# Optimization experiments

Hardware: AMD Instinct MI355X
Metric: run time of the kernel (lower is better)

## Reference

```python
import jax, jax.numpy as jnp
import numpy as np
import math

D_K = 64

def setup_inputs() -> dict:
    key = jax.random.key(0)
    kq, kk, kv, km = jax.random.split(key, 4)
    B, H, S, D = 4, 16, 2048, D_K
    Q = jax.random.normal(kq, (B, H, S, D), dtype=jnp.float32)
    K = jax.random.normal(kk, (B, H, S, D), dtype=jnp.float32)
    V = jax.random.normal(kv, (B, H, S, D), dtype=jnp.float32)
    attn_mask = jax.random.randint(km, (1, 1, S, S), 0, 2, dtype=jnp.int32)
    return {"Q": Q, "K": K, "V": V, "attn_mask": attn_mask}

def reference(Q, K, V, attn_mask):
    # scores: [B,H,S,S]
    scores = jnp.einsum('bhqd,bhkd->bhqk', Q, K) / math.sqrt(D_K)
    scores = jnp.where(attn_mask == 0, jnp.float32(-1e9), scores)
    attn = jax.nn.softmax(scores, axis=-1)
    context = jnp.einsum('bhqk,bhkd->bhqd', attn, V)
    return (context, attn)
```

## Files before the change

kernel.cpp:

```cpp
#include <hip/hip_runtime.h>
#include <hip/hip_bf16.h>
#include <stdint.h>

#define S_LEN 2048
#define DH    64
#define NBH   64
#define QR    128
#define KTI   64
#define NT    (S_LEN / KTI)
#define NTHR  512
#define SCALE2 (0.125f * 1.44269504f)
#define EXPB2  23.0f

using f32x4   = __attribute__((ext_vector_type(4))) float;
using short8v = __attribute__((ext_vector_type(8))) short;
using short4v = __attribute__((ext_vector_type(4))) short;

__device__ __forceinline__ short f2bf(float f) {
    union { float f; uint32_t u; } v; v.f = f;
    uint32_t u = v.u;
    return (short)((u + 0x7FFFu + ((u >> 16) & 1u)) >> 16);
}


__global__ void pack_mask_kernel(const int* __restrict__ mask, uint32_t* __restrict__ pmL) {
    int tid = blockIdx.x * 256 + threadIdx.x;
    int c  = tid & 15;
    int t  = (tid >> 4) & (NT - 1);
    int q4 = tid >> 9;
    uint32_t bits = 0;
    #pragma unroll
    for (int r = 0; r < 4; ++r)
        #pragma unroll
        for (int n = 0; n < 4; ++n) {
            int q = q4 * 4 + r;
            int k = t * KTI + n * 16 + c;
            if (mask[q * S_LEN + k]) bits |= 1u << (r * 4 + n);
        }
    pmL[tid] = bits;
}

__global__ void conv_k_kernel(const float* __restrict__ K, uint16_t* __restrict__ Kb) {
    size_t i = ((size_t)blockIdx.x * 256 + threadIdx.x) * 8;
    float4 a = *reinterpret_cast<const float4*>(K + i);
    float4 b = *reinterpret_cast<const float4*>(K + i + 4);
    short8v o;
    o[0] = f2bf(a.x); o[1] = f2bf(a.y); o[2] = f2bf(a.z); o[3] = f2bf(a.w);
    o[4] = f2bf(b.x); o[5] = f2bf(b.y); o[6] = f2bf(b.z); o[7] = f2bf(b.w);
    *reinterpret_cast<short8v*>(Kb + i) = o;
}

__global__ void trans_v_kernel(const float* __restrict__ V, uint16_t* __restrict__ Vt) {
    __shared__ short Ts[DH][72];
    int bh = blockIdx.x;
    int t  = blockIdx.y;
    const float* Vb = V + ((size_t)bh * S_LEN + t * KTI) * DH;
    int tid = threadIdx.x;
    #pragma unroll
    for (int i = 0; i < 4; ++i) {
        int lin = tid + i * 256;
        int row = lin >> 4;
        int c4  = (lin & 15) << 2;
        float4 v4 = *reinterpret_cast<const float4*>(Vb + row * DH + c4);
        Ts[c4 + 0][row] = f2bf(v4.x);
        Ts[c4 + 1][row] = f2bf(v4.y);
        Ts[c4 + 2][row] = f2bf(v4.z);
        Ts[c4 + 3][row] = f2bf(v4.w);
    }
    __syncthreads();
    #pragma unroll
    for (int i = 0; i < 2; ++i) {
        int lin = tid + i * 256;
        int d   = lin >> 3;
        int k8  = (lin & 7) << 3;
        short8v o = *reinterpret_cast<const short8v*>(&Ts[d][k8]);
        *reinterpret_cast<short8v*>(Vt + ((size_t)bh * DH + d) * S_LEN + t * KTI + k8) = o;
    }
}


__global__ __launch_bounds__(NTHR, 6)
void attn_kernel(const float* __restrict__ Q, const uint16_t* __restrict__ Kbf,
                 const uint16_t* __restrict__ VTb, const uint32_t* __restrict__ pmask,
                 float* __restrict__ outC, float* __restrict__ outA)
{
    __shared__ short Ks[2][KTI][72];
    __shared__ short VT[DH][72];
    __shared__ short Ps[8][16][72];

    const int wg  = blockIdx.x;
    const int k_  = wg >> 3;
    const int bh  = (wg & 7) * 8 + (k_ >> 4);
    const int q0  = (k_ & 15) * QR;

    const int tid = threadIdx.x;
    const int w   = tid >> 6;
    const int l   = tid & 63;
    const int l16 = l & 15;
    const int g   = l >> 4;
    const int srow = tid >> 3;
    const int scol = (tid & 7) << 3;

    const float*    Qb  = Q   + ((size_t)bh * S_LEN + q0) * DH;
    const uint16_t* Kbb = Kbf + (size_t)bh * S_LEN * DH;
    const uint16_t* Vbb = VTb + (size_t)bh * DH * S_LEN;
    float* Cb = outC + ((size_t)bh * S_LEN + q0) * DH;
    float* Ab = outA + (size_t)bh * S_LEN * S_LEN + (size_t)q0 * S_LEN;

    short8v aq0, aq1;
    {
        const float* qp = Qb + (w * 16 + l16) * DH;
        float4 a0 = *reinterpret_cast<const float4*>(qp + g * 8);
        float4 a1 = *reinterpret_cast<const float4*>(qp + g * 8 + 4);
        float4 a2 = *reinterpret_cast<const float4*>(qp + 32 + g * 8);
        float4 a3 = *reinterpret_cast<const float4*>(qp + 32 + g * 8 + 4);
        aq0[0] = f2bf(a0.x); aq0[1] = f2bf(a0.y); aq0[2] = f2bf(a0.z); aq0[3] = f2bf(a0.w);
        aq0[4] = f2bf(a1.x); aq0[5] = f2bf(a1.y); aq0[6] = f2bf(a1.z); aq0[7] = f2bf(a1.w);
        aq1[0] = f2bf(a2.x); aq1[1] = f2bf(a2.y); aq1[2] = f2bf(a2.z); aq1[3] = f2bf(a2.w);
        aq1[4] = f2bf(a3.x); aq1[5] = f2bf(a3.y); aq1[6] = f2bf(a3.z); aq1[7] = f2bf(a3.w);
    }

    const uint32_t* pmb = pmask + (size_t)((q0 >> 2) + (w << 2) + g) * (NT * 16) + l16;

    float ls[4] = {0.f, 0.f, 0.f, 0.f};
    {
        short8v kk = *reinterpret_cast<const short8v*>(Kbb + (size_t)srow * DH + scol);
        *reinterpret_cast<short8v*>(&Ks[0][srow][scol]) = kk;
    }
    __syncthreads();

    for (int t = 0; t < NT; ++t) {
        const int  cur  = t & 1;
        const bool more = (t + 1 < NT);
        short8v nk;
        if (more)
            nk = *reinterpret_cast<const short8v*>(Kbb + (size_t)((t + 1) * KTI + srow) * DH + scol);

        uint32_t mb = pmb[t << 4];

        f32x4 acc[4];
        #pragma unroll
        for (int n = 0; n < 4; ++n) {
            short8v b0 = *reinterpret_cast<const short8v*>(&Ks[cur][n * 16 + l16][g * 8]);
            short8v b1 = *reinterpret_cast<const short8v*>(&Ks[cur][n * 16 + l16][32 + g * 8]);
            f32x4 a = {0.f, 0.f, 0.f, 0.f};
            a = __builtin_amdgcn_mfma_f32_16x16x32_bf16(aq0, b0, a, 0, 0, 0);
            a = __builtin_amdgcn_mfma_f32_16x16x32_bf16(aq1, b1, a, 0, 0, 0);
            acc[n] = a;
        }

        #pragma unroll
        for (int n = 0; n < 4; ++n)
            #pragma unroll
            for (int r = 0; r < 4; ++r) {
                float e = __builtin_amdgcn_exp2f(acc[n][r] * SCALE2 - EXPB2);
                ls[r] += ((mb >> (r * 4 + n)) & 1u) ? e : 0.f;
            }

        if (more)
            *reinterpret_cast<short8v*>(&Ks[cur ^ 1][srow][scol]) = nk;
        __syncthreads();
    }

    float li[4];
    #pragma unroll
    for (int r = 0; r < 4; ++r) {
        float v = ls[r];
        v += __shfl_xor(v, 1);
        v += __shfl_xor(v, 2);
        v += __shfl_xor(v, 4);
        v += __shfl_xor(v, 8);
        li[r] = 1.0f / v;
    }

    f32x4 acco[4];
    #pragma unroll
    for (int n = 0; n < 4; ++n) acco[n] = (f32x4){0.f, 0.f, 0.f, 0.f};

    {
        short8v kk = *reinterpret_cast<const short8v*>(Kbb + (size_t)srow * DH + scol);
        *reinterpret_cast<short8v*>(&Ks[0][srow][scol]) = kk;
        short8v vv = *reinterpret_cast<const short8v*>(Vbb + (size_t)srow * S_LEN + scol);
        *reinterpret_cast<short8v*>(&VT[srow][scol]) = vv;
    }
    __syncthreads();

    for (int t = 0; t < NT; ++t) {
        const int  cur  = t & 1;
        const bool more = (t + 1 < NT);
        short8v nk, nv;
        if (more) {
            nk = *reinterpret_cast<const short8v*>(Kbb + (size_t)((t + 1) * KTI + srow) * DH + scol);
            nv = *reinterpret_cast<const short8v*>(Vbb + (size_t)srow * S_LEN + (t + 1) * KTI + scol);
        }
        uint32_t mb = pmb[t << 4];

        f32x4 acc[4];
        #pragma unroll
        for (int n = 0; n < 4; ++n) {
            short8v b0 = *reinterpret_cast<const short8v*>(&Ks[cur][n * 16 + l16][g * 8]);
            short8v b1 = *reinterpret_cast<const short8v*>(&Ks[cur][n * 16 + l16][32 + g * 8]);
            f32x4 a = {0.f, 0.f, 0.f, 0.f};
            a = __builtin_amdgcn_mfma_f32_16x16x32_bf16(aq0, b0, a, 0, 0, 0);
            a = __builtin_amdgcn_mfma_f32_16x16x32_bf16(aq1, b1, a, 0, 0, 0);
            acc[n] = a;
        }

        #pragma unroll
        for (int n = 0; n < 4; ++n)
            #pragma unroll
            for (int r = 0; r < 4; ++r) {
                float e = __builtin_amdgcn_exp2f(acc[n][r] * SCALE2 - EXPB2) * li[r];
                float p = ((mb >> (r * 4 + n)) & 1u) ? e : 0.0f;
                Ps[w][4 * g + r][n * 16 + l16] = f2bf(p);
            }

        asm volatile("" ::: "memory");

        {
            float* Aw = Ab + (size_t)(w * 16) * S_LEN + t * KTI;
            #pragma unroll
            for (int j = 0; j < 4; ++j) {
                int r4 = 4 * j + (l >> 4);
                short4v pv4 = *reinterpret_cast<const short4v*>(&Ps[w][r4][(l & 15) * 4]);
                f32x4 o;
                o[0] = __builtin_bit_cast(float, ((uint32_t)(uint16_t)pv4[0]) << 16);
                o[1] = __builtin_bit_cast(float, ((uint32_t)(uint16_t)pv4[1]) << 16);
                o[2] = __builtin_bit_cast(float, ((uint32_t)(uint16_t)pv4[2]) << 16);
                o[3] = __builtin_bit_cast(float, ((uint32_t)(uint16_t)pv4[3]) << 16);
                __builtin_nontemporal_store(o,
                    reinterpret_cast<f32x4*>(Aw + (size_t)r4 * S_LEN + (l & 15) * 4));
            }
        }

        short8v ap0 = *reinterpret_cast<const short8v*>(&Ps[w][l16][g * 8]);
        short8v ap1 = *reinterpret_cast<const short8v*>(&Ps[w][l16][32 + g * 8]);
        #pragma unroll
        for (int n = 0; n < 4; ++n) {
            short8v b0 = *reinterpret_cast<const short8v*>(&VT[n * 16 + l16][g * 8]);
            short8v b1 = *reinterpret_cast<const short8v*>(&VT[n * 16 + l16][32 + g * 8]);
            acco[n] = __builtin_amdgcn_mfma_f32_16x16x32_bf16(ap0, b0, acco[n], 0, 0, 0);
            acco[n] = __builtin_amdgcn_mfma_f32_16x16x32_bf16(ap1, b1, acco[n], 0, 0, 0);
        }

        if (more)
            *reinterpret_cast<short8v*>(&Ks[cur ^ 1][srow][scol]) = nk;
        __syncthreads();
        if (more)
            *reinterpret_cast<short8v*>(&VT[srow][scol]) = nv;
        __syncthreads();
    }

    #pragma unroll
    for (int n = 0; n < 4; ++n)
        #pragma unroll
        for (int r = 0; r < 4; ++r)
            Cb[(w * 16 + 4 * g + r) * DH + n * 16 + l16] = acco[n][r];
}

extern "C" void kernel_launch(void* const* d_in, const int* in_sizes, int n_in,
                              void* d_out, int out_size, void* d_ws, size_t ws_size,
                              hipStream_t stream)
{
    const float* Q    = (const float*)d_in[0];
    const float* K    = (const float*)d_in[1];
    const float* V    = (const float*)d_in[2];
    const int*   mask = (const int*)d_in[3];

    float* outC = (float*)d_out;
    float* outA = (float*)d_out + (size_t)NBH * S_LEN * DH;

    char* ws = (char*)d_ws;
    uint32_t* pmL = (uint32_t*)ws;
    uint16_t* Kbf = (uint16_t*)(ws + (1 << 20));
    uint16_t* VTb = (uint16_t*)(ws + (17 << 20));

    pack_mask_kernel<<<dim3((S_LEN / 4) * NT * 16 / 256), 256, 0, stream>>>(mask, pmL);
    conv_k_kernel<<<dim3((NBH * S_LEN * DH) / (256 * 8)), 256, 0, stream>>>(K, Kbf);
    trans_v_kernel<<<dim3(NBH, NT), 256, 0, stream>>>(V, VTb);
    attn_kernel<<<dim3(NBH * (S_LEN / QR)), NTHR, 0, stream>>>(Q, Kbf, VTb, pmL, outC, outA);
}
```

Before: 264.8 us.

## Swizzle LDS tiles, double-buffer V, and merge prep kernels into one launch

Replaces the padded 72-column shared-memory rows with an XOR-swizzled 64-column layout for the K, V and P tiles, which cuts LDS footprint and is meant to avoid bank conflicts. V is now double-buffered alongside K, so the second pass needs one barrier per tile instead of two. The three preprocessing kernels (K conversion, V transpose, mask packing) are fused into a single launch dispatched by block index, removing two launch gaps. The extra V buffer adds LDS, though the smaller row pitch offsets some of that. The main cost, the large fp32 attention-matrix write, is unchanged.

Result: slower. 272.7 us (+3.0%).

```diff
diff --git a/kernel.cpp b/kernel.cpp
--- a/kernel.cpp
+++ b/kernel.cpp
@@ -12,6 +12,8 @@
 #define SCALE2 (0.125f * 1.44269504f)
 #define EXPB2  23.0f
 
+#define SWZ(row, col) ((col) ^ (((row) & 7) << 3))
+
 using f32x4   = __attribute__((ext_vector_type(4))) float;
 using short8v = __attribute__((ext_vector_type(8))) short;
 using short4v = __attribute__((ext_vector_type(4))) short;
@@ -22,59 +24,67 @@
     return (short)((u + 0x7FFFu + ((u >> 16) & 1u)) >> 16);
 }
 
-
-__global__ void pack_mask_kernel(const int* __restrict__ mask, uint32_t* __restrict__ pmL) {
-    int tid = blockIdx.x * 256 + threadIdx.x;
-    int c  = tid & 15;
-    int t  = (tid >> 4) & (NT - 1);
-    int q4 = tid >> 9;
-    uint32_t bits = 0;
-    #pragma unroll
-    for (int r = 0; r < 4; ++r)
-        #pragma unroll
-        for (int n = 0; n < 4; ++n) {
-            int q = q4 * 4 + r;
-            int k = t * KTI + n * 16 + c;
-            if (mask[q * S_LEN + k]) bits |= 1u << (r * 4 + n);
-        }
-    pmL[tid] = bits;
-}
-
-__global__ void conv_k_kernel(const float* __restrict__ K, uint16_t* __restrict__ Kb) {
-    size_t i = ((size_t)blockIdx.x * 256 + threadIdx.x) * 8;
-    float4 a = *reinterpret_cast<const float4*>(K + i);
-    float4 b = *reinterpret_cast<const float4*>(K + i + 4);
-    short8v o;
-    o[0] = f2bf(a.x); o[1] = f2bf(a.y); o[2] = f2bf(a.z); o[3] = f2bf(a.w);
-    o[4] = f2bf(b.x); o[5] = f2bf(b.y); o[6] = f2bf(b.z); o[7] = f2bf(b.w);
-    *reinterpret_cast<short8v*>(Kb + i) = o;
-}
-
-__global__ void trans_v_kernel(const float* __restrict__ V, uint16_t* __restrict__ Vt) {
-    __shared__ short Ts[DH][72];
-    int bh = blockIdx.x;
-    int t  = blockIdx.y;
-    const float* Vb = V + ((size_t)bh * S_LEN + t * KTI) * DH;
-    int tid = threadIdx.x;
-    #pragma unroll
-    for (int i = 0; i < 4; ++i) {
-        int lin = tid + i * 256;
-        int row = lin >> 4;
-        int c4  = (lin & 15) << 2;
-        float4 v4 = *reinterpret_cast<const float4*>(Vb + row * DH + c4);
-        Ts[c4 + 0][row] = f2bf(v4.x);
-        Ts[c4 + 1][row] = f2bf(v4.y);
-        Ts[c4 + 2][row] = f2bf(v4.z);
-        Ts[c4 + 3][row] = f2bf(v4.w);
-    }
-    __syncthreads();
-    #pragma unroll
-    for (int i = 0; i < 2; ++i) {
-        int lin = tid + i * 256;
-        int d   = lin >> 3;
-        int k8  = (lin & 7) << 3;
-        short8v o = *reinterpret_cast<const short8v*>(&Ts[d][k8]);
-        *reinterpret_cast<short8v*>(Vt + ((size_t)bh * DH + d) * S_LEN + t * KTI + k8) = o;
+#define PREP_CONV_BLOCKS  4096
+#define PREP_TRANS_BLOCKS 2048
+#define PREP_MASK_BLOCKS  1024
+
+__global__ __launch_bounds__(256)
+void prep_kernel(const float* __restrict__ K, const float* __restrict__ V,
+                 const int* __restrict__ mask,
+                 uint16_t* __restrict__ Kb, uint16_t* __restrict__ Vt,
+                 uint32_t* __restrict__ pmL)
+{
+    const int b = blockIdx.x;
+    if (b < PREP_CONV_BLOCKS) {
+        size_t i = ((size_t)b * 256 + threadIdx.x) * 8;
+        float4 a = *reinterpret_cast<const float4*>(K + i);
+        float4 c = *reinterpret_cast<const float4*>(K + i + 4);
+        short8v o;
+        o[0] = f2bf(a.x); o[1] = f2bf(a.y); o[2] = f2bf(a.z); o[3] = f2bf(a.w);
+        o[4] = f2bf(c.x); o[5] = f2bf(c.y); o[6] = f2bf(c.z); o[7] = f2bf(c.w);
+        *reinterpret_cast<short8v*>(Kb + i) = o;
+    } else if (b < PREP_CONV_BLOCKS + PREP_TRANS_BLOCKS) {
+        __shared__ short Ts[DH][72];
+        int b2 = b - PREP_CONV_BLOCKS;
+        int bh = b2 >> 5;
+        int t  = b2 & 31;
+        const float* Vb = V + ((size_t)bh * S_LEN + t * KTI) * DH;
+        int tid = threadIdx.x;
+        #pragma unroll
+        for (int i = 0; i < 4; ++i) {
+            int lin = tid + i * 256;
+            int row = lin >> 4;
+            int c4  = (lin & 15) << 2;
+            float4 v4 = *reinterpret_cast<const float4*>(Vb + row * DH + c4);
+            Ts[c4 + 0][row] = f2bf(v4.x);
+            Ts[c4 + 1][row] = f2bf(v4.y);
+            Ts[c4 + 2][row] = f2bf(v4.z);
+            Ts[c4 + 3][row] = f2bf(v4.w);
+        }
+        __syncthreads();
+        #pragma unroll
+        for (int i = 0; i < 2; ++i) {
+            int lin = tid + i * 256;
+            int d   = lin >> 3;
+            int k8  = (lin & 7) << 3;
+            short8v o = *reinterpret_cast<const short8v*>(&Ts[d][k8]);
+            *reinterpret_cast<short8v*>(Vt + ((size_t)bh * DH + d) * S_LEN + t * KTI + k8) = o;
+        }
+    } else {
+        int tid = (b - PREP_CONV_BLOCKS - PREP_TRANS_BLOCKS) * 256 + threadIdx.x;
+        int c  = tid & 15;
+        int t  = (tid >> 4) & (NT - 1);
+        int q4 = tid >> 9;
+        uint32_t bits = 0;
+        #pragma unroll
+        for (int r = 0; r < 4; ++r)
+            #pragma unroll
+            for (int n = 0; n < 4; ++n) {
+                int q = q4 * 4 + r;
+                int k = t * KTI + n * 16 + c;
+                if (mask[q * S_LEN + k]) bits |= 1u << (r * 4 + n);
+            }
+        pmL[tid] = bits;
     }
 }
 
@@ -84,9 +94,9 @@
                  const uint16_t* __restrict__ VTb, const uint32_t* __restrict__ pmask,
                  float* __restrict__ outC, float* __restrict__ outA)
 {
-    __shared__ short Ks[2][KTI][72];
-    __shared__ short VT[DH][72];
-    __shared__ short Ps[8][16][72];
+    __shared__ short Ks[2][KTI][64];
+    __shared__ short VT[2][DH][64];
+    __shared__ short Ps[8][16][64];
 
     const int wg  = blockIdx.x;
     const int k_  = wg >> 3;
@@ -100,6 +110,7 @@
     const int g   = l >> 4;
     const int srow = tid >> 3;
     const int scol = (tid & 7) << 3;
+    const int sscol = SWZ(srow, scol);
 
     const float*    Qb  = Q   + ((size_t)bh * S_LEN + q0) * DH;
     const uint16_t* Kbb = Kbf + (size_t)bh * S_LEN * DH;
@@ -122,10 +133,13 @@
 
     const uint32_t* pmb = pmask + (size_t)((q0 >> 2) + (w << 2) + g) * (NT * 16) + l16;
 
+    const int bc0 = SWZ(l16, g * 8);
+    const int bc1 = SWZ(l16, 32 + g * 8);
+
     float ls[4] = {0.f, 0.f, 0.f, 0.f};
     {
         short8v kk = *reinterpret_cast<const short8v*>(Kbb + (size_t)srow * DH + scol);
-        *reinterpret_cast<short8v*>(&Ks[0][srow][scol]) = kk;
+        *reinterpret_cast<short8v*>(&Ks[0][srow][sscol]) = kk;
     }
     __syncthreads();
 
@@ -141,8 +155,8 @@
         f32x4 acc[4];
         #pragma unroll
         for (int n = 0; n < 4; ++n) {
-            short8v b0 = *reinterpret_cast<const short8v*>(&Ks[cur][n * 16 + l16][g * 8]);
-            short8v b1 = *reinterpret_cast<const short8v*>(&Ks[cur][n * 16 + l16][32 + g * 8]);
+            short8v b0 = *reinterpret_cast<const short8v*>(&Ks[cur][n * 16 + l16][bc0]);
+            short8v b1 = *reinterpret_cast<const short8v*>(&Ks[cur][n * 16 + l16][bc1]);
             f32x4 a = {0.f, 0.f, 0.f, 0.f};
             a = __builtin_amdgcn_mfma_f32_16x16x32_bf16(aq0, b0, a, 0, 0, 0);
             a = __builtin_amdgcn_mfma_f32_16x16x32_bf16(aq1, b1, a, 0, 0, 0);
@@ -158,7 +172,7 @@
             }
 
         if (more)
-            *reinterpret_cast<short8v*>(&Ks[cur ^ 1][srow][scol]) = nk;
+            *reinterpret_cast<short8v*>(&Ks[cur ^ 1][srow][sscol]) = nk;
         __syncthreads();
     }
 
@@ -179,9 +193,9 @@
 
     {
         short8v kk = *reinterpret_cast<const short8v*>(Kbb + (size_t)srow * DH + scol);
-        *reinterpret_cast<short8v*>(&Ks[0][srow][scol]) = kk;
+        *reinterpret_cast<short8v*>(&Ks[0][srow][sscol]) = kk;
         short8v vv = *reinterpret_cast<const short8v*>(Vbb + (size_t)srow * S_LEN + scol);
-        *reinterpret_cast<short8v*>(&VT[srow][scol]) = vv;
+        *reinterpret_cast<short8v*>(&VT[0][srow][sscol]) = vv;
     }
     __syncthreads();
 
@@ -198,8 +212,8 @@
         f32x4 acc[4];
         #pragma unroll
         for (int n = 0; n < 4; ++n) {
-            short8v b0 = *reinterpret_cast<const short8v*>(&Ks[cur][n * 16 + l16][g * 8]);
-            short8v b1 = *reinterpret_cast<const short8v*>(&Ks[cur][n * 16 + l16][32 + g * 8]);
+            short8v b0 = *reinterpret_cast<const short8v*>(&Ks[cur][n * 16 + l16][bc0]);
+            short8v b1 = *reinterpret_cast<const short8v*>(&Ks[cur][n * 16 + l16][bc1]);
             f32x4 a = {0.f, 0.f, 0.f, 0.f};
             a = __builtin_amdgcn_mfma_f32_16x16x32_bf16(aq0, b0, a, 0, 0, 0);
             a = __builtin_amdgcn_mfma_f32_16x16x32_bf16(aq1, b1, a, 0, 0, 0);
@@ -212,7 +226,7 @@
             for (int r = 0; r < 4; ++r) {
                 float e = __builtin_amdgcn_exp2f(acc[n][r] * SCALE2 - EXPB2) * li[r];
                 float p = ((mb >> (r * 4 + n)) & 1u) ? e : 0.0f;
-                Ps[w][4 * g + r][n * 16 + l16] = f2bf(p);
+                Ps[w][4 * g + r][SWZ(4 * g + r, n * 16 + l16)] = f2bf(p);
             }
 
         asm volatile("" ::: "memory");
@@ -222,7 +236,8 @@
             #pragma unroll
             for (int j = 0; j < 4; ++j) {
                 int r4 = 4 * j + (l >> 4);
-                short4v pv4 = *reinterpret_cast<const short4v*>(&Ps[w][r4][(l & 15) * 4]);
+                short4v pv4 = *reinterpret_cast<const short4v*>(
+                    &Ps[w][r4][SWZ(r4, (l & 15) * 4)]);
                 f32x4 o;
                 o[0] = __builtin_bit_cast(float, ((uint32_t)(uint16_t)pv4[0]) << 16);
                 o[1] = __builtin_bit_cast(float, ((uint32_t)(uint16_t)pv4[1]) << 16);
@@ -233,21 +248,20 @@
             }
         }
 
-        short8v ap0 = *reinterpret_cast<const short8v*>(&Ps[w][l16][g * 8]);
-        short8v ap1 = *reinterpret_cast<const short8v*>(&Ps[w][l16][32 + g * 8]);
+        short8v ap0 = *reinterpret_cast<const short8v*>(&Ps[w][l16][bc0]);
+        short8v ap1 = *reinterpret_cast<const short8v*>(&Ps[w][l16][bc1]);
         #pragma unroll
         for (int n = 0; n < 4; ++n) {
-            short8v b0 = *reinterpret_cast<const short8v*>(&VT[n * 16 + l16][g * 8]);
-            short8v b1 = *reinterpret_cast<const short8v*>(&VT[n * 16 + l16][32 + g * 8]);
+            short8v b0 = *reinterpret_cast<const short8v*>(&VT[cur][n * 16 + l16][bc0]);
+            short8v b1 = *reinterpret_cast<const short8v*>(&VT[cur][n * 16 + l16][bc1]);
             acco[n] = __builtin_amdgcn_mfma_f32_16x16x32_bf16(ap0, b0, acco[n], 0, 0, 0);
             acco[n] = __builtin_amdgcn_mfma_f32_16x16x32_bf16(ap1, b1, acco[n], 0, 0, 0);
         }
 
-        if (more)
-            *reinterpret_cast<short8v*>(&Ks[cur ^ 1][srow][scol]) = nk;
-        __syncthreads();
-        if (more)
-            *reinterpret_cast<short8v*>(&VT[srow][scol]) = nv;
+        if (more) {
+            *reinterpret_cast<short8v*>(&Ks[cur ^ 1][srow][sscol]) = nk;
+            *reinterpret_cast<short8v*>(&VT[cur ^ 1][srow][sscol]) = nv;
+        }
         __syncthreads();
     }
 
@@ -275,8 +289,7 @@
     uint16_t* Kbf = (uint16_t*)(ws + (1 << 20));
     uint16_t* VTb = (uint16_t*)(ws + (17 << 20));
 
-    pack_mask_kernel<<<dim3((S_LEN / 4) * NT * 16 / 256), 256, 0, stream>>>(mask, pmL);
-    conv_k_kernel<<<dim3((NBH * S_LEN * DH) / (256 * 8)), 256, 0, stream>>>(K, Kbf);
-    trans_v_kernel<<<dim3(NBH, NT), 256, 0, stream>>>(V, VTb);
+    prep_kernel<<<dim3(PREP_CONV_BLOCKS + PREP_TRANS_BLOCKS + PREP_MASK_BLOCKS),
+                  256, 0, stream>>>(K, V, mask, Kbf, VTb, pmL);
     attn_kernel<<<dim3(NBH * (S_LEN / QR)), NTHR, 0, stream>>>(Q, Kbf, VTb, pmL, outC, outA);
 }
```
